# Kernel tuning notes

Measured on AMD Instinct MI355X. Metric: run time of the kernel, lower is better.

## Reference

```python
import jax, jax.numpy as jnp
import numpy as np

TOP_K = 2
LORA_SCALE = 32.0 / 16.0  # alpha / r


def setup_inputs() -> dict:
    key = jax.random.key(0)
    ks = jax.random.split(key, 11)
    B, S, H, I, E, R = 4, 2048, 2048, 5504, 8, 16
    s = lambda k, shape, fan: jax.random.normal(k, shape, jnp.float32) / np.sqrt(fan)
    return {
        "x": jax.random.normal(ks[0], (B, S, H), jnp.float32),
        "gate_values": jax.random.normal(ks[1], (B, E), jnp.float32),
        "Wg": s(ks[2], (I, H), H),
        "Ag": s(ks[3], (E, H, R), H),
        "Bg": s(ks[4], (E, R, I), R),
        "Wu": s(ks[5], (I, H), H),
        "Au": s(ks[6], (E, H, R), H),
        "Bu": s(ks[7], (E, R, I), R),
        "Wd": s(ks[8], (H, I), I),
        "Ad": s(ks[9], (E, I, R), I),
        "Bd": s(ks[10], (E, R, H), R),
    }


def _top_k_binary_gates(gate_values, k):
    # set top-k entries per row to 1.0, others 0.0 (bsz, num_experts)
    _, idx = jax.lax.top_k(gate_values, k)
    b = jnp.zeros_like(gate_values)
    rows = jnp.arange(gate_values.shape[0])[:, None]
    return b.at[rows, idx].set(1.0)


def _adapter_linear(x, W, A, B, binary_gates):
    # base: (b,s,in) @ (out,in)^T -> (b,s,out)
    base = jnp.einsum("bsh,oh->bso", x, W)
    # per-expert LoRA: gate e * x @ A_e @ B_e, summed over selected experts
    u = jnp.einsum("bsh,ehr->bser", x, A)            # (b,s,E,r) low-rank
    delta = jnp.einsum("bser,ero,be->bso", u, B, binary_gates)
    return base + LORA_SCALE * delta


def reference(x, gate_values, Wg, Ag, Bg, Wu, Au, Bu, Wd, Ad, Bd):
    g = _top_k_binary_gates(gate_values, TOP_K)
    gate_out = _adapter_linear(x, Wg, Ag, Bg, g)
    up_out = _adapter_linear(x, Wu, Au, Bu, g)
    h = jax.nn.silu(gate_out) * up_out              # SwiGLU
    return _adapter_linear(h, Wd, Ad, Bd, g)
```

## Files before the change

### kernel.cpp

```cpp
#include <hip/hip_runtime.h>
#include <stdint.h>

typedef unsigned short u16;
typedef __bf16 bf16x8 __attribute__((ext_vector_type(8)));
typedef float f32x4 __attribute__((ext_vector_type(4)));

#define AS1 __attribute__((address_space(1)))
#define AS3 __attribute__((address_space(3)))

__device__ __forceinline__ void g2l16(const void* g, void* l) {
  __builtin_amdgcn_global_load_lds((AS1 void*)(void*)g, (AS3 void*)l, 16, 0, 0);
}

__device__ __forceinline__ u16 f2bf(float f) {
  union { float f; uint32_t u; } v; v.f = f;
  return (u16)((v.u + 0x7fffu + ((v.u >> 16) & 1u)) >> 16);
}
__device__ __forceinline__ float bf2f(u16 b) {
  union { uint32_t u; float f; } v; v.u = ((uint32_t)b) << 16;
  return v.f;
}

__device__ __forceinline__ bf16x8 dsr(uint32_t a) {
  bf16x8 r;
  asm volatile("ds_read_b128 %0, %1" : "=v"(r) : "v"(a));
  return r;
}
__device__ __forceinline__ void barx() {
  __builtin_amdgcn_sched_barrier(0);
  __builtin_amdgcn_s_barrier();
  __builtin_amdgcn_sched_barrier(0);
}
#define LGKM0 do { asm volatile("s_waitcnt lgkmcnt(0)" ::: "memory"); \
                   __builtin_amdgcn_sched_barrier(0); } while (0)
#define VMCNT(n) asm volatile("s_waitcnt vmcnt(" #n ")" ::: "memory")

__global__ void k_top2(const float* __restrict__ gv, int* __restrict__ idx) {
  int b = threadIdx.x;
  if (b < 4) {
    const float* g = gv + b * 8;
    int i1 = 0; float v1 = g[0];
    for (int e = 1; e < 8; ++e) if (g[e] > v1) { v1 = g[e]; i1 = e; }
    int i2 = -1; float v2 = -3.0e38f;
    for (int e = 0; e < 8; ++e) if (e != i1 && g[e] > v2) { v2 = g[e]; i2 = e; }
    idx[2 * b] = i1; idx[2 * b + 1] = i2;
  }
}

__global__ void k_cast(const float* __restrict__ in, u16* __restrict__ out, int n4) {
  int i = blockIdx.x * 256 + threadIdx.x;
  if (i < n4) {
    float4 v = ((const float4*)in)[i];
    ushort4 o = make_ushort4(f2bf(v.x), f2bf(v.y), f2bf(v.z), f2bf(v.w));
    ((ushort4*)out)[i] = o;
  }
}

__global__ void k_cast2d(const float* __restrict__ in, u16* __restrict__ out,
                         int Rs, int Cs, int total4, int Co) {
  int i = blockIdx.x * 256 + threadIdx.x;
  if (i >= total4) return;
  size_t e0 = (size_t)i * 4;
  int c = (int)(e0 % Co);
  int r = (int)(e0 / Co);
  ushort4 o;
  if (r < Rs && c + 3 < Cs) {
    float4 v = *(const float4*)(in + (size_t)r * Cs + c);
    o = make_ushort4(f2bf(v.x), f2bf(v.y), f2bf(v.z), f2bf(v.w));
  } else {
    u16 a[4];
    #pragma unroll
    for (int k = 0; k < 4; ++k)
      a[k] = (r < Rs && c + k < Cs) ? f2bf(in[(size_t)r * Cs + c + k]) : (u16)0;
    o = make_ushort4(a[0], a[1], a[2], a[3]);
  }
  *(ushort4*)(out + e0) = o;
}

__global__ void k_aT(const float* __restrict__ A0, const float* __restrict__ A1,
                     const int* __restrict__ idx, u16* __restrict__ out,
                     int Kd, int jmax) {
  int t = blockIdx.x * 256 + threadIdx.x;
  if (t >= 4 * jmax * Kd) return;
  int h = t % Kd;
  int j = (t / Kd) % jmax;
  int b = t / (Kd * jmax);
  const float* src = (j >= 32) ? A1 : A0;
  int jj = j & 31;
  int e = idx[2 * b + ((jj >> 4) & 1)];
  int r = jj & 15;
  out[t] = f2bf(src[((size_t)e * Kd + h) * 16 + r]);
}

__global__ void k_bT(const float* __restrict__ Bsrc, const int* __restrict__ idx,
                     u16* __restrict__ out, int Nout, int Nsrc) {
  int t = blockIdx.x * 256 + threadIdx.x;
  if (t < 4 * Nout * 32) {
    int j = t & 31;
    int n = (t >> 5) % Nout;
    int b = t / (Nout * 32);
    int e = (j & 16) ? idx[2 * b + 1] : idx[2 * b];
    int r = j & 15;
    out[t] = (n < Nsrc) ? f2bf(Bsrc[((size_t)e * 16 + r) * Nsrc + n]) : (u16)0;
  }
}

template <int N2>
__global__ __launch_bounds__(256) void k_skinny(
    const u16* __restrict__ A, const u16* __restrict__ BT,
    float* __restrict__ part, int M, int lda, int K, int total_iters,
    int iters_per_chunk) {
  __shared__ u16 sA[128 * 64];
  __shared__ u16 sB[N2 * 64];
  int nm = M >> 7;
  int bm = blockIdx.x % nm, chunk = blockIdx.x / nm;
  int m0 = bm << 7;
  int batch = m0 >> 11;
  int tid = threadIdx.x, lane = tid & 63, w = tid >> 6;
  int kb = chunk * iters_per_chunk;
  int ke = min(total_iters, kb + iters_per_chunk);

  const u16* Bb = BT + (size_t)batch * N2 * K;

  const u16* ga[4]; u16* la[4];
  #pragma unroll
  for (int t = 0; t < 4; ++t) {
    int cb = 4 * w + t;
    int q = cb * 64 + lane;
    int row = q >> 3;
    int c = (q & 7) ^ (row & 7);
    ga[t] = A + (size_t)(m0 + row) * lda + (size_t)kb * 64 + c * 8;
    la[t] = sA + cb * 512;
  }
  constexpr int nB = N2 / 32;
  const u16* gb[nB]; u16* lb[nB];
  #pragma unroll
  for (int t = 0; t < nB; ++t) {
    int cb = nB * w + t;
    int q = cb * 64 + lane;
    int row = q >> 3;
    int c = (q & 7) ^ (row & 7);
    gb[t] = Bb + (size_t)row * K + (size_t)kb * 64 + c * 8;
    lb[t] = sB + cb * 512;
  }

  f32x4 acc[2][N2 / 16] = {};
  for (int kt = kb; kt < ke; ++kt) {
    #pragma unroll
    for (int t = 0; t < 4; ++t) { g2l16(ga[t], la[t]); ga[t] += 64; }
    #pragma unroll
    for (int t = 0; t < nB; ++t) { g2l16(gb[t], lb[t]); gb[t] += 64; }
    __syncthreads();
    #pragma unroll
    for (int ks = 0; ks < 2; ++ks) {
      int cb0 = ks * 4 + (lane >> 4);
      bf16x8 af[2], bfr[N2 / 16];
      #pragma unroll
      for (int mi = 0; mi < 2; ++mi) {
        int row = 32 * w + mi * 16 + (lane & 15);
        af[mi] = *(const bf16x8*)(sA + (row * 8 + (cb0 ^ (row & 7))) * 8);
      }
      #pragma unroll
      for (int ni = 0; ni < N2 / 16; ++ni) {
        int row = ni * 16 + (lane & 15);
        bfr[ni] = *(const bf16x8*)(sB + (row * 8 + (cb0 ^ (row & 7))) * 8);
      }
      #pragma unroll
      for (int mi = 0; mi < 2; ++mi)
        #pragma unroll
        for (int ni = 0; ni < N2 / 16; ++ni)
          acc[mi][ni] = __builtin_amdgcn_mfma_f32_16x16x32_bf16(
              af[mi], bfr[ni], acc[mi][ni], 0, 0, 0);
    }
    __syncthreads();
  }

  int rb = (lane >> 4) * 4, cc = lane & 15;
  #pragma unroll
  for (int mi = 0; mi < 2; ++mi)
    #pragma unroll
    for (int ni = 0; ni < N2 / 16; ++ni)
      #pragma unroll
      for (int reg = 0; reg < 4; ++reg) {
        int gr = m0 + 32 * w + mi * 16 + rb + reg;
        int gc = ni * 16 + cc;
        part[((size_t)chunk * M + gr) * N2 + gc] = acc[mi][ni][reg];
      }
}

__global__ void k_fin(const float* __restrict__ part, u16* __restrict__ out0,
                      u16* __restrict__ out1, int M, int N2, int nch) {
  int t = blockIdx.x * 256 + threadIdx.x;
  if (t >= M * N2) return;
  float s = 0.f;
  for (int c = 0; c < nch; ++c) s += part[(size_t)c * M * N2 + t];
  int j = t % N2, bs = t / N2;
  u16 v = f2bf(2.0f * s);
  if (N2 == 64) {
    if (j < 32) out0[(size_t)bs * 32 + j] = v;
    else        out1[(size_t)bs * 32 + (j - 32)] = v;
  } else {
    out0[(size_t)bs * 32 + j] = v;
  }
}

__global__ __launch_bounds__(512, 2)
void k_gemm256(const u16* __restrict__ A, const u16* __restrict__ Bm,
               const u16* __restrict__ A2, const u16* __restrict__ B2,
               const u16* __restrict__ Gprev, void* __restrict__ Out,
               int N, int K, int mode) {
  __shared__ u16 lds[65536];
  int nt = N >> 8;
  int nm = gridDim.x / nt;
  int perx = nm >> 3;
  int xcd = blockIdx.x & 7;
  int v = blockIdx.x >> 3;
  int bn = v / perx;
  int bm = xcd * perx + (v - bn * perx);
  int m0 = bm << 8, n0 = bn << 8;
  int batch = m0 >> 11;

  int tid = threadIdx.x;
  int lane = tid & 63, w = tid >> 6;
  int wm = w >> 2, wn = w & 3;
  int g = lane >> 4, l7 = lane & 7, l15 = lane & 15;

  int srow = w * 8 + (lane >> 3);
  int scol = ((lane & 7) ^ (lane >> 3)) * 8;
  const u16* pA = A + (size_t)(m0 + srow) * K + scol;
  const u16* pB = Bm + (size_t)(n0 + srow) * K + scol;

  uint32_t Lb = (uint32_t)(uint64_t)(&lds[0]);
  uint32_t aTh0 = (uint32_t)(wm * 8192 + l15 * 128 + ((g ^ l7) * 16));
  uint32_t aTh1 = aTh0 ^ 64;
  uint32_t bTh0 = (uint32_t)(wn * 4096 + l15 * 128 + ((g ^ l7) * 16));
  uint32_t bTh1 = bTh0 ^ 64;

  f32x4 acc[2][4][2][2] = {};
  bf16x8 af[4][2], bfr[2][2];

  int kiters = K >> 6;

#define STAGE_A(h1, jt_) do { \
    u16* _d = lds + (((jt_) & 1) << 14) + ((h1) * 8192) + (w << 9); \
    const u16* _s = pA + (size_t)((h1) * 128) * K + (((size_t)(jt_)) << 6); \
    g2l16(_s, _d); \
    g2l16(_s + (size_t)64 * K, _d + 4096); \
  } while (0)
#define STAGE_B(h1, jt_) do { \
    u16* _d = lds + 32768 + (((jt_) & 1) << 14) + ((h1) * 8192) + (w << 9); \
    const u16* _s = pB + (size_t)((h1) * 128) * K + (((size_t)(jt_)) << 6); \
    g2l16(_s, _d); \
    g2l16(_s + (size_t)64 * K, _d + 4096); \
  } while (0)
#define LDA(mh, bufb) do { \
    uint32_t _b = Lb + (bufb) + (mh) * 16384; \
    _Pragma("unroll") for (int mi = 0; mi < 4; ++mi) { \
      af[mi][0] = dsr(_b + aTh0 + mi * 2048); \
      af[mi][1] = dsr(_b + aTh1 + mi * 2048); \
    } } while (0)
#define LDB(nh, bufb) do { \
    uint32_t _b = Lb + 65536 + (bufb) + (nh) * 16384; \
    _Pragma("unroll") for (int ni = 0; ni < 2; ++ni) { \
      bfr[ni][0] = dsr(_b + bTh0 + ni * 2048); \
      bfr[ni][1] = dsr(_b + bTh1 + ni * 2048); \
    } } while (0)
#define MFMA_Q(mh, nh) do { \
    __builtin_amdgcn_s_setprio(1); \
    _Pragma("unroll") for (int ks = 0; ks < 2; ++ks) \
      _Pragma("unroll") for (int mi = 0; mi < 4; ++mi) \
        _Pragma("unroll") for (int ni = 0; ni < 2; ++ni) \
          acc[mh][mi][nh][ni] = __builtin_amdgcn_mfma_f32_16x16x32_bf16( \
              af[mi][ks], bfr[ni][ks], acc[mh][mi][nh][ni], 0, 0, 0); \
    __builtin_amdgcn_s_setprio(0); \
  } while (0)

  STAGE_A(0, 0); STAGE_A(1, 0); STAGE_B(0, 0); STAGE_B(1, 0);
  STAGE_A(0, 1); STAGE_A(1, 1);
  VMCNT(4);
  barx();

  int jt = 0;
  for (; jt < kiters - 2; ++jt) {
    uint32_t bufb = (uint32_t)((jt & 1) << 15);
    LDA(0, bufb); LDB(0, bufb);
    STAGE_B(0, jt + 1);
    barx(); LGKM0; MFMA_Q(0, 0); barx();
    LDB(1, bufb);
    STAGE_B(1, jt + 1);
    barx(); LGKM0; MFMA_Q(0, 1); barx();
    LDA(1, bufb);
    STAGE_A(0, jt + 2);
    barx(); LGKM0; MFMA_Q(1, 1); barx();
    LDB(0, bufb);
    STAGE_A(1, jt + 2);
    VMCNT(4);
    barx(); LGKM0; MFMA_Q(1, 0); barx();
  }
  {
    uint32_t bufb = (uint32_t)((jt & 1) << 15);
    LDA(0, bufb); LDB(0, bufb);
    STAGE_B(0, kiters - 1);
    barx(); LGKM0; MFMA_Q(0, 0); barx();
    LDB(1, bufb);
    STAGE_B(1, kiters - 1);
    barx(); LGKM0; MFMA_Q(0, 1); barx();
    LDA(1, bufb);
    barx(); LGKM0; MFMA_Q(1, 1); barx();
    LDB(0, bufb);
    VMCNT(0);
    barx(); LGKM0; MFMA_Q(1, 0); barx();
  }
  {
    uint32_t bufb = (uint32_t)(((kiters - 1) & 1) << 15);
    LDA(0, bufb); LDB(0, bufb); LGKM0; MFMA_Q(0, 0);
    LDB(1, bufb); LGKM0; MFMA_Q(0, 1);
    LDA(1, bufb); LGKM0; MFMA_Q(1, 1);
    LDB(0, bufb); LGKM0; MFMA_Q(1, 0);
  }

  {
    const u16* B2b = B2 + (size_t)batch * N * 32;
    int srow2 = w * 16 + (lane >> 2);
    int scol2 = ((lane & 3) ^ ((lane >> 2) & 3)) * 8;
    const u16* pA2 = A2 + (size_t)(m0 + srow2) * 32 + scol2;
    const u16* pB2 = B2b + (size_t)(n0 + srow2) * 32 + scol2;
    barx();
    {
      u16* dA = lds + (w << 9);
      g2l16(pA2, dA); g2l16(pA2 + 4096, dA + 4096);
      u16* dB = lds + 32768 + (w << 9);
      g2l16(pB2, dB); g2l16(pB2 + 4096, dB + 4096);
    }
    VMCNT(0);
    barx();
    uint32_t c2 = (uint32_t)((g ^ (lane & 3)) * 16);
    bf16x8 af2[4], bf2[2];
    #pragma unroll
    for (int mh = 0; mh < 2; ++mh) {
      #pragma unroll
      for (int mi = 0; mi < 4; ++mi)
        af2[mi] = dsr(Lb + mh * 8192 + wm * 4096 + mi * 1024 + l15 * 64 + c2);
      #pragma unroll
      for (int nh = 0; nh < 2; ++nh) {
        bf2[0] = dsr(Lb + 65536 + nh * 8192 + wn * 2048 + l15 * 64 + c2);
        bf2[1] = dsr(Lb + 65536 + nh * 8192 + wn * 2048 + 1024 + l15 * 64 + c2);
        LGKM0;
        #pragma unroll
        for (int mi = 0; mi < 4; ++mi)
          #pragma unroll
          for (int ni = 0; ni < 2; ++ni)
            acc[mh][mi][nh][ni] = __builtin_amdgcn_mfma_f32_16x16x32_bf16(
                af2[mi], bf2[ni], acc[mh][mi][nh][ni], 0, 0, 0);
      }
    }
  }

  int rb = (lane >> 4) * 4, cc = lane & 15;
  #pragma unroll
  for (int mh = 0; mh < 2; ++mh)
    #pragma unroll
    for (int mi = 0; mi < 4; ++mi)
      #pragma unroll
      for (int nh = 0; nh < 2; ++nh)
        #pragma unroll
        for (int ni = 0; ni < 2; ++ni)
          #pragma unroll
          for (int reg = 0; reg < 4; ++reg) {
            int gr = m0 + mh * 128 + wm * 64 + mi * 16 + rb + reg;
            int gc = n0 + nh * 128 + wn * 32 + ni * 16 + cc;
            size_t pos = (size_t)gr * N + gc;
            float vv = acc[mh][mi][nh][ni][reg];
            if (mode == 0) {
              vv = vv / (1.f + __expf(-vv));
              ((u16*)Out)[pos] = f2bf(vv);
            } else if (mode == 1) {
              float gg = bf2f(Gprev[pos]);
              ((u16*)Out)[pos] = f2bf(gg * vv);
            } else {
              ((float*)Out)[pos] = vv;
            }
          }
#undef STAGE_A
#undef STAGE_B
#undef LDA
#undef LDB
#undef MFMA_Q
}

extern "C" void kernel_launch(void* const* d_in, const int* in_sizes, int n_in,
                              void* d_out, int out_size, void* d_ws, size_t ws_size,
                              hipStream_t stream) {
  const float* x  = (const float*)d_in[0];
  const float* gv = (const float*)d_in[1];
  const float* Wg = (const float*)d_in[2];
  const float* Ag = (const float*)d_in[3];
  const float* Bg = (const float*)d_in[4];
  const float* Wu = (const float*)d_in[5];
  const float* Au = (const float*)d_in[6];
  const float* Bu = (const float*)d_in[7];
  const float* Wd = (const float*)d_in[8];
  const float* Ad = (const float*)d_in[9];
  const float* Bd = (const float*)d_in[10];
  float* out = (float*)d_out;

  char* ws = (char*)d_ws;
  size_t off = 0;
  auto alloc = [&](size_t bytes) -> void* {
    void* p = ws + off;
    off = (off + bytes + 255) & ~(size_t)255;
    return p;
  };
  int* idx  = (int*)alloc(32);
  u16* xb   = (u16*)alloc((size_t)8192 * 2048 * 2);
  u16* Wgb  = (u16*)alloc((size_t)5632 * 2048 * 2);
  u16* Wub  = (u16*)alloc((size_t)5632 * 2048 * 2);
  u16* xag  = (u16*)alloc((size_t)8192 * 32 * 2);
  u16* xau  = (u16*)alloc((size_t)8192 * 32 * 2);
  u16* ha   = (u16*)alloc((size_t)8192 * 32 * 2);
  u16* BgT  = (u16*)alloc((size_t)4 * 5632 * 32 * 2);
  u16* BuT  = (u16*)alloc((size_t)4 * 5632 * 32 * 2);
  u16* BdT  = (u16*)alloc((size_t)4 * 2048 * 32 * 2);
  u16* AxT  = (u16*)alloc((size_t)4 * 64 * 2048 * 2);
  u16* AdT  = (u16*)alloc((size_t)4 * 32 * 5504 * 2);
  u16* gbuf = (u16*)alloc((size_t)8192 * 5632 * 2);
  if (off > ws_size) return;

  u16* Wdb = Wub;
  float* part_xa = (float*)gbuf;
  float* part_ha = (float*)Wgb;

  k_top2<<<1, 64, 0, stream>>>(gv, idx);
  k_cast<<<16384, 256, 0, stream>>>(x, xb, 4194304);
  k_cast2d<<<11264, 256, 0, stream>>>(Wg, Wgb, 5504, 2048, 2883584, 2048);
  k_cast2d<<<11264, 256, 0, stream>>>(Wu, Wub, 5504, 2048, 2883584, 2048);
  k_aT<<<2048, 256, 0, stream>>>(Ag, Au, idx, AxT, 2048, 64);
  k_aT<<<2752, 256, 0, stream>>>(Ad, Ad, idx, AdT, 5504, 32);
  k_bT<<<2816, 256, 0, stream>>>(Bg, idx, BgT, 5632, 5504);
  k_bT<<<2816, 256, 0, stream>>>(Bu, idx, BuT, 5632, 5504);
  k_bT<<<1024, 256, 0, stream>>>(Bd, idx, BdT, 2048, 2048);

  k_skinny<64><<<64 * 4, 256, 0, stream>>>(xb, AxT, part_xa, 8192, 2048, 2048, 32, 8);
  k_fin<<<2048, 256, 0, stream>>>(part_xa, xag, xau, 8192, 64, 4);

  k_gemm256<<<32 * 22, 512, 0, stream>>>(xb, Wgb, xag, BgT, (const u16*)nullptr,
                                         gbuf, 5632, 2048, 0);
  k_gemm256<<<32 * 22, 512, 0, stream>>>(xb, Wub, xau, BuT, gbuf,
                                         gbuf, 5632, 2048, 1);

  k_cast2d<<<11264, 256, 0, stream>>>(Wd, Wdb, 2048, 5504, 2883584, 5632);

  k_skinny<32><<<64 * 4, 256, 0, stream>>>(gbuf, AdT, part_ha, 8192, 5632, 5504, 86, 22);
  k_fin<<<1024, 256, 0, stream>>>(part_ha, ha, ha, 8192, 32, 4);

  k_gemm256<<<32 * 8, 512, 0, stream>>>(gbuf, Wdb, ha, BdT, (const u16*)nullptr,
                                        out, 2048, 5632, 2);
}
```

Baseline: 912.6 us.

## Unroll GEMM main loop by two with immediate LDS offsets and B-fragment reuse

Unrolls the K loop by two so the double-buffer offsets become compile-time immediates in ds_read_b128, which removes per-read address arithmetic. B fragments are now held in two register sets, so the fourth quadrant reuses the first B fragment without rereading LDS. It also deepens the global-to-LDS staging schedule: B tiles are issued earlier, the vmcnt threshold changes, and one barrier pair is removed per iteration. In exchange it raises register pressure, and the reworked prefetch ordering assumes an even K-iteration count, which could race or misbehave if that assumption is wrong.

Result: no change. 900.4 us (-1.3%).

```diff
diff --git a/kernel.cpp b/kernel.cpp
--- a/kernel.cpp
+++ b/kernel.cpp
@@ -21,6 +21,12 @@
   return v.f;
 }
 
+template <int OFF>
+__device__ __forceinline__ bf16x8 dsrO(uint32_t a) {
+  bf16x8 r;
+  asm volatile("ds_read_b128 %0, %1 offset:%2" : "=v"(r) : "v"(a), "n"(OFF));
+  return r;
+}
 __device__ __forceinline__ bf16x8 dsr(uint32_t a) {
   bf16x8 r;
   asm volatile("ds_read_b128 %0, %1" : "=v"(r) : "v"(a));
@@ -231,13 +237,13 @@
   const u16* pB = Bm + (size_t)(n0 + srow) * K + scol;
 
   uint32_t Lb = (uint32_t)(uint64_t)(&lds[0]);
-  uint32_t aTh0 = (uint32_t)(wm * 8192 + l15 * 128 + ((g ^ l7) * 16));
-  uint32_t aTh1 = aTh0 ^ 64;
-  uint32_t bTh0 = (uint32_t)(wn * 4096 + l15 * 128 + ((g ^ l7) * 16));
-  uint32_t bTh1 = bTh0 ^ 64;
+  uint32_t bA0 = Lb + (uint32_t)(wm * 8192 + l15 * 128 + ((g ^ l7) * 16));
+  uint32_t bA1 = bA0 ^ 64;
+  uint32_t bB0 = Lb + 65536u + (uint32_t)(wn * 4096 + l15 * 128 + ((g ^ l7) * 16));
+  uint32_t bB1 = bB0 ^ 64;
 
   f32x4 acc[2][4][2][2] = {};
-  bf16x8 af[4][2], bfr[2][2];
+  bf16x8 af[4][2], b0f[2][2], b1f[2][2];
 
   int kiters = K >> 6;
 
@@ -253,70 +259,84 @@
     g2l16(_s, _d); \
     g2l16(_s + (size_t)64 * K, _d + 4096); \
   } while (0)
-#define LDA(mh, bufb) do { \
-    uint32_t _b = Lb + (bufb) + (mh) * 16384; \
-    _Pragma("unroll") for (int mi = 0; mi < 4; ++mi) { \
-      af[mi][0] = dsr(_b + aTh0 + mi * 2048); \
-      af[mi][1] = dsr(_b + aTh1 + mi * 2048); \
-    } } while (0)
-#define LDB(nh, bufb) do { \
-    uint32_t _b = Lb + 65536 + (bufb) + (nh) * 16384; \
-    _Pragma("unroll") for (int ni = 0; ni < 2; ++ni) { \
-      bfr[ni][0] = dsr(_b + bTh0 + ni * 2048); \
-      bfr[ni][1] = dsr(_b + bTh1 + ni * 2048); \
-    } } while (0)
-#define MFMA_Q(mh, nh) do { \
+#define LDA_IMM(mh, BUF) do { \
+    af[0][0] = dsrO<(BUF)*32768 + (mh)*16384 + 0>(bA0); \
+    af[0][1] = dsrO<(BUF)*32768 + (mh)*16384 + 0>(bA1); \
+    af[1][0] = dsrO<(BUF)*32768 + (mh)*16384 + 2048>(bA0); \
+    af[1][1] = dsrO<(BUF)*32768 + (mh)*16384 + 2048>(bA1); \
+    af[2][0] = dsrO<(BUF)*32768 + (mh)*16384 + 4096>(bA0); \
+    af[2][1] = dsrO<(BUF)*32768 + (mh)*16384 + 4096>(bA1); \
+    af[3][0] = dsrO<(BUF)*32768 + (mh)*16384 + 6144>(bA0); \
+    af[3][1] = dsrO<(BUF)*32768 + (mh)*16384 + 6144>(bA1); \
+  } while (0)
+#define LDB_IMM(dst, nh, BUF) do { \
+    dst[0][0] = dsrO<(BUF)*32768 + (nh)*16384 + 0>(bB0); \
+    dst[0][1] = dsrO<(BUF)*32768 + (nh)*16384 + 0>(bB1); \
+    dst[1][0] = dsrO<(BUF)*32768 + (nh)*16384 + 2048>(bB0); \
+    dst[1][1] = dsrO<(BUF)*32768 + (nh)*16384 + 2048>(bB1); \
+  } while (0)
+#define MFMA_Q(mh, nh, BF) do { \
     __builtin_amdgcn_s_setprio(1); \
     _Pragma("unroll") for (int ks = 0; ks < 2; ++ks) \
       _Pragma("unroll") for (int mi = 0; mi < 4; ++mi) \
         _Pragma("unroll") for (int ni = 0; ni < 2; ++ni) \
           acc[mh][mi][nh][ni] = __builtin_amdgcn_mfma_f32_16x16x32_bf16( \
-              af[mi][ks], bfr[ni][ks], acc[mh][mi][nh][ni], 0, 0, 0); \
+              af[mi][ks], BF[ni][ks], acc[mh][mi][nh][ni], 0, 0, 0); \
     __builtin_amdgcn_s_setprio(0); \
   } while (0)
 
+#define TILE_BODY(BUF, jt_) do { \
+     \
+    LDA_IMM(0, BUF); \
+    LDB_IMM(b0f, 0, BUF); \
+    STAGE_B(1, (jt_) + 1); \
+    barx(); LGKM0; MFMA_Q(0, 0, b0f); barx(); \
+     \
+    LDB_IMM(b1f, 1, BUF); \
+    STAGE_A(0, (jt_) + 2); \
+    barx(); LGKM0; MFMA_Q(0, 1, b1f); barx(); \
+     \
+    LDA_IMM(1, BUF); \
+    STAGE_B(0, (jt_) + 2); \
+    barx(); LGKM0; MFMA_Q(1, 1, b1f); barx(); \
+     \
+    STAGE_A(1, (jt_) + 2); \
+    MFMA_Q(1, 0, b0f); \
+    VMCNT(6); \
+    barx(); \
+  } while (0)
+
   STAGE_A(0, 0); STAGE_A(1, 0); STAGE_B(0, 0); STAGE_B(1, 0);
-  STAGE_A(0, 1); STAGE_A(1, 1);
-  VMCNT(4);
+  STAGE_A(0, 1); STAGE_B(0, 1); STAGE_A(1, 1);
+  VMCNT(6);
   barx();
 
-  int jt = 0;
-  for (; jt < kiters - 2; ++jt) {
-    uint32_t bufb = (uint32_t)((jt & 1) << 15);
-    LDA(0, bufb); LDB(0, bufb);
-    STAGE_B(0, jt + 1);
-    barx(); LGKM0; MFMA_Q(0, 0); barx();
-    LDB(1, bufb);
-    STAGE_B(1, jt + 1);
-    barx(); LGKM0; MFMA_Q(0, 1); barx();
-    LDA(1, bufb);
-    STAGE_A(0, jt + 2);
-    barx(); LGKM0; MFMA_Q(1, 1); barx();
-    LDB(0, bufb);
-    STAGE_A(1, jt + 2);
-    VMCNT(4);
-    barx(); LGKM0; MFMA_Q(1, 0); barx();
+  for (int jt = 0; jt + 3 < kiters; jt += 2) {
+    TILE_BODY(0, jt);
+    TILE_BODY(1, jt + 1);
   }
   {
-    uint32_t bufb = (uint32_t)((jt & 1) << 15);
-    LDA(0, bufb); LDB(0, bufb);
-    STAGE_B(0, kiters - 1);
-    barx(); LGKM0; MFMA_Q(0, 0); barx();
-    LDB(1, bufb);
+    LDA_IMM(0, 0);
+    LDB_IMM(b0f, 0, 0);
     STAGE_B(1, kiters - 1);
-    barx(); LGKM0; MFMA_Q(0, 1); barx();
-    LDA(1, bufb);
-    barx(); LGKM0; MFMA_Q(1, 1); barx();
-    LDB(0, bufb);
+    barx(); LGKM0; MFMA_Q(0, 0, b0f); barx();
+    LDB_IMM(b1f, 1, 0);
+    barx(); LGKM0; MFMA_Q(0, 1, b1f); barx();
+    LDA_IMM(1, 0);
+    barx(); LGKM0; MFMA_Q(1, 1, b1f); barx();
+    MFMA_Q(1, 0, b0f);
     VMCNT(0);
-    barx(); LGKM0; MFMA_Q(1, 0); barx();
+    barx();
   }
   {
-    uint32_t bufb = (uint32_t)(((kiters - 1) & 1) << 15);
-    LDA(0, bufb); LDB(0, bufb); LGKM0; MFMA_Q(0, 0);
-    LDB(1, bufb); LGKM0; MFMA_Q(0, 1);
-    LDA(1, bufb); LGKM0; MFMA_Q(1, 1);
-    LDB(0, bufb); LGKM0; MFMA_Q(1, 0);
+    LDA_IMM(0, 1);
+    LDB_IMM(b0f, 0, 1);
+    LGKM0; MFMA_Q(0, 0, b0f);
+    LDB_IMM(b1f, 1, 1);
+    LGKM0; MFMA_Q(0, 1, b1f);
+    LDA_IMM(1, 1);
+    LGKM0; MFMA_Q(1, 1, b1f);
+    MFMA_Q(1, 0, b0f);
   }
 
   {
@@ -383,9 +403,10 @@
           }
 #undef STAGE_A
 #undef STAGE_B
-#undef LDA
-#undef LDB
+#undef LDA_IMM
+#undef LDB_IMM
 #undef MFMA_Q
+#undef TILE_BODY
 }
 
 extern "C" void kernel_launch(void* const* d_in, const int* in_sizes, int n_in,
```
